# Kernel optimization log

Hardware: AMD Instinct MI355X
Metric: run time of the kernel (lower is better)

The kernel has to match this reference:

```python
import jax, jax.numpy as jnp
import numpy as np
import math

N_HEAD = 16

def setup_inputs() -> dict:
    key = jax.random.key(0)
    ks = jax.random.split(key, 5)
    B, T, C = 4, 2048, 1024
    x = jax.random.normal(ks[0], (B, T, C), dtype=jnp.float32)
    # xavier-uniform-ish scale for dense kernels
    W_attn = jax.random.normal(ks[1], (C, 3 * C), dtype=jnp.float32) * (1.0 / math.sqrt(C))
    b_attn = jnp.zeros((3 * C,), dtype=jnp.float32)
    W_proj = jax.random.normal(ks[2], (C, C), dtype=jnp.float32) * (1.0 / math.sqrt(C))
    b_proj = jnp.zeros((C,), dtype=jnp.float32)
    return {"x": x, "W_attn": W_attn, "b_attn": b_attn, "W_proj": W_proj, "b_proj": b_proj}

def reference(x, W_attn, b_attn, W_proj, b_proj):
    B, T, C = x.shape
    H = N_HEAD
    D = C // H
    qkv = x @ W_attn + b_attn                      # [B,T,3C]
    q, k, v = jnp.split(qkv, 3, axis=-1)
    q = q.reshape(B, T, H, D).transpose(0, 2, 1, 3)  # [B,H,T,D]
    k = k.reshape(B, T, H, D).transpose(0, 2, 1, 3)
    v = v.reshape(B, T, H, D).transpose(0, 2, 1, 3)
    att = jnp.einsum("bhqd,bhkd->bhqk", q, k) * (1.0 / math.sqrt(D))  # [B,H,T,T]
    causal = jnp.tril(jnp.ones((T, T), dtype=bool))
    att = jnp.where(causal, att, jnp.float32(-jnp.inf))
    att = jax.nn.softmax(att, axis=-1)             # exp(att - logsumexp)
    # dropout rates are 0.0 -> identity
    y = jnp.einsum("bhqk,bhkd->bhqd", att, v)      # [B,H,T,D]
    y = y.transpose(0, 2, 1, 3).reshape(B, T, C)
    y = y @ W_proj + b_proj
    return y
```

## Files before the change

### kernel.cpp

```cpp
#include <hip/hip_runtime.h>
#include <hip/hip_bf16.h>

typedef short s16x8 __attribute__((ext_vector_type(8)));
typedef float f32x4 __attribute__((ext_vector_type(4)));
typedef float f32x2 __attribute__((ext_vector_type(2)));

#define MFMA_BF16(A, B, C) __builtin_amdgcn_mfma_f32_16x16x32_bf16(A, B, C, 0, 0, 0)

constexpr int Bn = 4, Tn = 2048, Cn = 1024, Hn = 16, Dn = 64;
constexpr int Mn = Bn * Tn;
constexpr int Nqkv = 3 * Cn;
constexpr float SC = 0.125f * 1.44269504089f;

__device__ __forceinline__ ushort f2bfu(float f) {
    __hip_bfloat16 h = __float2bfloat16(f);
    return *reinterpret_cast<ushort*>(&h);
}
__device__ __forceinline__ uint pkbf(float a, float b) {
    __hip_bfloat162 h = __float22bfloat162_rn(make_float2(a, b));
    return *reinterpret_cast<uint*>(&h);
}

__device__ __forceinline__ f32x2 pk_add(f32x2 a, f32x2 b) {
    f32x2 d; asm("v_pk_add_f32 %0, %1, %2" : "=v"(d) : "v"(a), "v"(b)); return d;
}
__device__ __forceinline__ f32x2 pk_mul(f32x2 a, f32x2 b) {
    f32x2 d; asm("v_pk_mul_f32 %0, %1, %2" : "=v"(d) : "v"(a), "v"(b)); return d;
}

__device__ __forceinline__ void gl_lds16(const void* g, void* l) {
    __builtin_amdgcn_global_load_lds(
        (const __attribute__((address_space(1))) void*)(uintptr_t)g,
        (__attribute__((address_space(3))) void*)(uint32_t)(uintptr_t)l,
        16, 0, 0);
}

__global__ __launch_bounds__(256) void conv_bf16_kernel(
    const float* __restrict__ src, ushort* __restrict__ dst, int n4)
{
    int i = blockIdx.x * blockDim.x + threadIdx.x;
    int stride = gridDim.x * blockDim.x;
    for (; i < n4; i += stride) {
        float4 v = ((const float4*)src)[i];
        ushort4 o;
        o.x = f2bfu(v.x); o.y = f2bfu(v.y); o.z = f2bfu(v.z); o.w = f2bfu(v.w);
        ((ushort4*)dst)[i] = o;
    }
}

__global__ __launch_bounds__(256) void transpose_cvt_kernel(
    const float* __restrict__ W, ushort* __restrict__ Wt, int K, int N)
{
    __shared__ __align__(16) float Ls[64][68];
    const int t = threadIdx.x;
    const int n0 = blockIdx.x * 64, k0 = blockIdx.y * 64;
#pragma unroll
    for (int p = 0; p < 4; ++p) {
        int r = (t >> 4) + p * 16;
        int c = (t & 15) * 4;
        *(float4*)&Ls[r][c] = *(const float4*)&W[(size_t)(k0 + r) * N + n0 + c];
    }
    __syncthreads();
    const int n = t >> 2;
    const int ks = (t & 3) * 16;
    union { ushort s[16]; uint4 u[2]; } tmp;
#pragma unroll
    for (int j = 0; j < 16; ++j) tmp.s[j] = f2bfu(Ls[ks + j][n]);
    uint4* dp = (uint4*)&Wt[(size_t)(n0 + n) * K + k0 + ks];
    dp[0] = tmp.u[0];
    dp[1] = tmp.u[1];
}

__global__ __launch_bounds__(256) void qkv_gemm_mfma(
    const ushort* __restrict__ A, const ushort* __restrict__ Bt,
    const float* __restrict__ bias,
    ushort* __restrict__ Qo, ushort* __restrict__ Ko, ushort* __restrict__ Vo)
{
    __shared__ __align__(16) ushort As[128 * 64];
    __shared__ __align__(16) ushort Bs[128 * 64];
    const int tid = threadIdx.x;
    const int m0 = blockIdx.x * 128, n0 = blockIdx.y * 128;
    const int w = tid >> 6, lane = tid & 63, l15 = lane & 15, qd = lane >> 4;
    const int wm = (w >> 1) * 64, wn = (w & 1) * 64;
    const int lrow = lane >> 3;
    const int lchunk = (lane & 7) ^ (lrow & 7);

    const ushort* gA = A + (size_t)(m0 + w * 32 + lrow) * Cn + lchunk * 8;
    const ushort* gB = Bt + (size_t)(n0 + w * 32 + lrow) * Cn + lchunk * 8;
    ushort* lA = &As[(w * 32) * 64];
    ushort* lB = &Bs[(w * 32) * 64];

    f32x4 acc[4][4] = {};
    const bool isV = (n0 >= 2 * Cn);

    if (!isV) {
        for (int k0 = 0; k0 < Cn; k0 += 64) {
            __syncthreads();
#pragma unroll
            for (int t = 0; t < 4; ++t) {
                gl_lds16(gA + (size_t)t * 8 * Cn + k0, lA + t * 8 * 64);
                gl_lds16(gB + (size_t)t * 8 * Cn + k0, lB + t * 8 * 64);
            }
            __syncthreads();
#pragma unroll
            for (int ks = 0; ks < 2; ++ks) {
                const int xs = (((ks * 4 + qd) ^ (l15 & 7))) * 8;
                s16x8 af[4], bfr[4];
#pragma unroll
                for (int i = 0; i < 4; ++i) {
                    af[i]  = *(const s16x8*)&As[(wm + i * 16 + l15) * 64 + xs];
                    bfr[i] = *(const s16x8*)&Bs[(wn + i * 16 + l15) * 64 + xs];
                }
#pragma unroll
                for (int mt = 0; mt < 4; ++mt)
#pragma unroll
                    for (int nt = 0; nt < 4; ++nt)
                        acc[mt][nt] = MFMA_BF16(af[mt], bfr[nt], acc[mt][nt]);
            }
        }
        const int sel = n0 >> 10;
        ushort* O = (sel == 0) ? Qo : Ko;
        const float scl = (sel == 0) ? SC : 1.0f;
#pragma unroll
        for (int nt = 0; nt < 4; ++nt) {
            const int n_g = n0 + wn + nt * 16 + l15;
            const float bv = bias[n_g];
            const int h = (n_g >> 6) & 15;
            const int d = n_g & 63;
#pragma unroll
            for (int mt = 0; mt < 4; ++mt) {
#pragma unroll
                for (int r = 0; r < 4; ++r) {
                    const int m_g = m0 + wm + mt * 16 + qd * 4 + r;
                    const int b = m_g >> 11, t = m_g & 2047;
                    O[(((size_t)(b * Hn + h) * Tn + t) << 6) + d] =
                        f2bfu((acc[mt][nt][r] + bv) * scl);
                }
            }
        }
    } else {
        for (int k0 = 0; k0 < Cn; k0 += 64) {
            __syncthreads();
#pragma unroll
            for (int t = 0; t < 4; ++t) {
                gl_lds16(gA + (size_t)t * 8 * Cn + k0, lA + t * 8 * 64);
                gl_lds16(gB + (size_t)t * 8 * Cn + k0, lB + t * 8 * 64);
            }
            __syncthreads();
#pragma unroll
            for (int ks = 0; ks < 2; ++ks) {
                const int xs = (((ks * 4 + qd) ^ (l15 & 7))) * 8;
                s16x8 af[4], bfr[4];
#pragma unroll
                for (int i = 0; i < 4; ++i) {
                    af[i]  = *(const s16x8*)&As[(wm + i * 16 + l15) * 64 + xs];
                    bfr[i] = *(const s16x8*)&Bs[(wn + i * 16 + l15) * 64 + xs];
                }
#pragma unroll
                for (int mt = 0; mt < 4; ++mt)
#pragma unroll
                    for (int nt = 0; nt < 4; ++nt)
                        acc[nt][mt] = MFMA_BF16(bfr[nt], af[mt], acc[nt][mt]);
            }
        }
#pragma unroll
        for (int nt = 0; nt < 4; ++nt) {
            const int n_b = n0 + wn + nt * 16 + qd * 4;
            const float4 bv = *(const float4*)&bias[n_b];
            const int h = (n_b >> 6) & 15;
            const int d0 = n_b & 63;
#pragma unroll
            for (int mt = 0; mt < 4; ++mt) {
                const int m_g = m0 + wm + mt * 16 + l15;
                const int b = m_g >> 11, tt = m_g & 2047;
                const size_t rowb = (size_t)(b * Hn + h) * Dn;
                Vo[(rowb + d0 + 0) * Tn + tt] = f2bfu(acc[nt][mt][0] + bv.x);
                Vo[(rowb + d0 + 1) * Tn + tt] = f2bfu(acc[nt][mt][1] + bv.y);
                Vo[(rowb + d0 + 2) * Tn + tt] = f2bfu(acc[nt][mt][2] + bv.z);
                Vo[(rowb + d0 + 3) * Tn + tt] = f2bfu(acc[nt][mt][3] + bv.w);
            }
        }
    }
}

__global__ __launch_bounds__(256, 4) void attn_mfma(
    const ushort* __restrict__ Q, const ushort* __restrict__ K,
    const ushort* __restrict__ Vt, ushort* __restrict__ Y)
{
    __shared__ __align__(16) ushort Ks[2][64 * 64];
    __shared__ __align__(16) ushort Vs[2][64 * 64];
    __shared__ __align__(16) ushort Ps[64 * 64];

    const int tid = threadIdx.x;
    const int bh = blockIdx.x, bx = blockIdx.y;
    const int w = tid >> 6, lane = tid & 63, l15 = lane & 15, qd = lane >> 4;
    const size_t base = (size_t)bh * Tn * Dn;
    const int lrow = lane >> 3;
    const int lchunk = (lane & 7) ^ (lrow & 7);
    const int q_l = w * 16 + l15;
    const int frow = q_l * 64;
    const int fx0 = ((0 * 4 + qd) ^ (l15 & 7)) * 8;
    const int fx1 = ((1 * 4 + qd) ^ (l15 & 7)) * 8;
    const int b = bh >> 4, h = bh & 15;

    const ushort* Kg = K + base + (size_t)(w * 16 + lrow) * Dn + lchunk * 8;
    const ushort* Vg = Vt + base + (size_t)(w * 16 + lrow) * Tn + lchunk * 8;
    const ushort* Qp = Q + base + (size_t)l15 * Dn + qd * 8;

#pragma unroll
    for (int half = 0; half < 2; ++half) {
        const int qt = half ? (31 - bx) : bx;

        const ushort* qrow = Qp + (size_t)(qt * 64 + w * 16) * Dn;
        s16x8 qf0 = *(const s16x8*)(qrow);
        s16x8 qf1 = *(const s16x8*)(qrow + 32);

        __syncthreads();
#pragma unroll
        for (int t = 0; t < 2; ++t) {
            gl_lds16(Kg + (size_t)(t * 8) * Dn, &Ks[0][(w * 16 + t * 8) * 64]);
            gl_lds16(Vg + (size_t)(t * 8) * Tn, &Vs[0][(w * 16 + t * 8) * 64]);
        }

        float m_run = -1e30f, l_run = 0.f;
        f32x4 o[4] = {};

        for (int kt = 0; kt <= qt; ++kt) {
            const int buf = kt & 1;
            __syncthreads();
            if (kt < qt) {
#pragma unroll
                for (int t = 0; t < 2; ++t) {
                    gl_lds16(Kg + (size_t)((kt + 1) * 64 + t * 8) * Dn,
                             &Ks[buf ^ 1][(w * 16 + t * 8) * 64]);
                    gl_lds16(Vg + (size_t)(t * 8) * Tn + (kt + 1) * 64,
                             &Vs[buf ^ 1][(w * 16 + t * 8) * 64]);
                }
            }

            f32x4 s[4] = {};
            __builtin_amdgcn_s_setprio(1);
#pragma unroll
            for (int nt = 0; nt < 4; ++nt) {
                s16x8 kf = *(const s16x8*)&Ks[buf][(nt * 16 + l15) * 64 + fx0];
                s[nt] = MFMA_BF16(kf, qf0, s[nt]);
            }
#pragma unroll
            for (int nt = 0; nt < 4; ++nt) {
                s16x8 kf = *(const s16x8*)&Ks[buf][(nt * 16 + l15) * 64 + fx1];
                s[nt] = MFMA_BF16(kf, qf1, s[nt]);
            }
            __builtin_amdgcn_s_setprio(0);

            if (kt == qt) {
#pragma unroll
                for (int nt = 0; nt < 4; ++nt)
#pragma unroll
                    for (int r = 0; r < 4; ++r)
                        if (nt * 16 + qd * 4 + r > q_l) s[nt][r] = -1e30f;
            }

            float a0 = fmaxf(fmaxf(s[0][0], s[0][1]), fmaxf(s[0][2], s[0][3]));
            float a1 = fmaxf(fmaxf(s[1][0], s[1][1]), fmaxf(s[1][2], s[1][3]));
            float a2 = fmaxf(fmaxf(s[2][0], s[2][1]), fmaxf(s[2][2], s[2][3]));
            float a3 = fmaxf(fmaxf(s[3][0], s[3][1]), fmaxf(s[3][2], s[3][3]));
            float mx = fmaxf(fmaxf(a0, a1), fmaxf(a2, a3));
            mx = fmaxf(mx, __shfl_xor(mx, 16));
            mx = fmaxf(mx, __shfl_xor(mx, 32));

            if (!__all(mx <= m_run + 8.f)) {
                float m_new = fmaxf(m_run, mx);
                float alpha = exp2f(m_run - m_new);
                m_run = m_new;
                l_run *= alpha;
                f32x2 aa = {alpha, alpha};
#pragma unroll
                for (int dt = 0; dt < 4; ++dt) {
                    o[dt].lo = pk_mul(o[dt].lo, aa);
                    o[dt].hi = pk_mul(o[dt].hi, aa);
                }
            }

            const f32x2 negm = {-m_run, -m_run};
            f32x2 lac0 = {0.f, 0.f}, lac1 = {0.f, 0.f};
#pragma unroll
            for (int nt = 0; nt < 4; ++nt) {
                s[nt].lo = pk_add(s[nt].lo, negm);
                s[nt].hi = pk_add(s[nt].hi, negm);
                s[nt][0] = exp2f(s[nt][0]);
                s[nt][1] = exp2f(s[nt][1]);
                s[nt][2] = exp2f(s[nt][2]);
                s[nt][3] = exp2f(s[nt][3]);
                lac0 = pk_add(lac0, s[nt].lo);
                lac1 = pk_add(lac1, s[nt].hi);
            }
            lac0 = pk_add(lac0, lac1);
            l_run += lac0[0] + lac0[1];

#pragma unroll
            for (int nt = 0; nt < 4; ++nt) {
                uint2 pk;
                pk.x = pkbf(s[nt][0], s[nt][1]);
                pk.y = pkbf(s[nt][2], s[nt][3]);
                const int pc = 2 * nt + (qd >> 1), po = (qd & 1) * 4;
                *(uint2*)&Ps[frow + ((pc ^ (l15 & 7)) * 8) + po] = pk;
            }

            {
                s16x8 pb = *(const s16x8*)&Ps[frow + fx0];
                __builtin_amdgcn_s_setprio(1);
#pragma unroll
                for (int dt = 0; dt < 4; ++dt) {
                    s16x8 vf = *(const s16x8*)&Vs[buf][(dt * 16 + l15) * 64 + fx0];
                    o[dt] = MFMA_BF16(vf, pb, o[dt]);
                }
                pb = *(const s16x8*)&Ps[frow + fx1];
#pragma unroll
                for (int dt = 0; dt < 4; ++dt) {
                    s16x8 vf = *(const s16x8*)&Vs[buf][(dt * 16 + l15) * 64 + fx1];
                    o[dt] = MFMA_BF16(vf, pb, o[dt]);
                }
                __builtin_amdgcn_s_setprio(0);
            }
        }

        float lt = l_run;
        lt += __shfl_xor(lt, 16);
        lt += __shfl_xor(lt, 32);
        const float inv = 1.f / lt;
        const int t_g = qt * 64 + w * 16 + l15;
        ushort* yp = Y + ((size_t)(b * Tn + t_g)) * Cn + h * Dn + qd * 4;
#pragma unroll
        for (int dt = 0; dt < 4; ++dt) {
            uint2 pk;
            pk.x = pkbf(o[dt][0] * inv, o[dt][1] * inv);
            pk.y = pkbf(o[dt][2] * inv, o[dt][3] * inv);
            *(uint2*)(yp + dt * 16) = pk;
        }
    }
}

__global__ __launch_bounds__(256) void proj_gemm_mfma(
    const ushort* __restrict__ A, const ushort* __restrict__ Bt,
    const float* __restrict__ bias, float* __restrict__ out)
{
    __shared__ __align__(16) ushort As[128 * 64];
    __shared__ __align__(16) ushort Bs[128 * 64];
    const int tid = threadIdx.x;
    const int m0 = blockIdx.x * 128, n0 = blockIdx.y * 128;
    const int w = tid >> 6, lane = tid & 63, l15 = lane & 15, qd = lane >> 4;
    const int wm = (w >> 1) * 64, wn = (w & 1) * 64;
    const int lrow = lane >> 3;
    const int lchunk = (lane & 7) ^ (lrow & 7);

    const ushort* gA = A + (size_t)(m0 + w * 32 + lrow) * Cn + lchunk * 8;
    const ushort* gB = Bt + (size_t)(n0 + w * 32 + lrow) * Cn + lchunk * 8;
    ushort* lA = &As[(w * 32) * 64];
    ushort* lB = &Bs[(w * 32) * 64];

    f32x4 acc[4][4] = {};

    for (int k0 = 0; k0 < Cn; k0 += 64) {
        __syncthreads();
#pragma unroll
        for (int t = 0; t < 4; ++t) {
            gl_lds16(gA + (size_t)t * 8 * Cn + k0, lA + t * 8 * 64);
            gl_lds16(gB + (size_t)t * 8 * Cn + k0, lB + t * 8 * 64);
        }
        __syncthreads();
#pragma unroll
        for (int ks = 0; ks < 2; ++ks) {
            const int xs = (((ks * 4 + qd) ^ (l15 & 7))) * 8;
            s16x8 af[4], bfr[4];
#pragma unroll
            for (int i = 0; i < 4; ++i) {
                af[i]  = *(const s16x8*)&As[(wm + i * 16 + l15) * 64 + xs];
                bfr[i] = *(const s16x8*)&Bs[(wn + i * 16 + l15) * 64 + xs];
            }
#pragma unroll
            for (int mt = 0; mt < 4; ++mt)
#pragma unroll
                for (int nt = 0; nt < 4; ++nt)
                    acc[mt][nt] = MFMA_BF16(af[mt], bfr[nt], acc[mt][nt]);
        }
    }

#pragma unroll
    for (int nt = 0; nt < 4; ++nt) {
        int n_g = n0 + wn + nt * 16 + l15;
        float bv = bias[n_g];
#pragma unroll
        for (int mt = 0; mt < 4; ++mt) {
#pragma unroll
            for (int r = 0; r < 4; ++r) {
                int m_g = m0 + wm + mt * 16 + qd * 4 + r;
                out[(size_t)m_g * Cn + n_g] = acc[mt][nt][r] + bv;
            }
        }
    }
}

extern "C" void kernel_launch(void* const* d_in, const int* in_sizes, int n_in,
                              void* d_out, int out_size, void* d_ws, size_t ws_size,
                              hipStream_t stream) {
    const float* x      = (const float*)d_in[0];
    const float* W_attn = (const float*)d_in[1];
    const float* b_attn = (const float*)d_in[2];
    const float* W_proj = (const float*)d_in[3];
    const float* b_proj = (const float*)d_in[4];
    float* out = (float*)d_out;

    constexpr size_t PER = (size_t)Mn * Cn;
    ushort* Qb  = (ushort*)d_ws;
    ushort* Kb  = Qb + PER;
    ushort* Vtb = Kb + PER;
    ushort* Yb  = Vtb + PER;

    ushort* WtA  = (ushort*)d_out;
    ushort* x_bf = WtA + (size_t)Nqkv * Cn;
    ushort* WtP  = Qb;

    conv_bf16_kernel<<<1024, 256, 0, stream>>>(x, x_bf, (int)(PER / 4));
    transpose_cvt_kernel<<<dim3(Nqkv / 64, Cn / 64), 256, 0, stream>>>(
        W_attn, WtA, Cn, Nqkv);
    qkv_gemm_mfma<<<dim3(Mn / 128, Nqkv / 128), 256, 0, stream>>>(
        x_bf, WtA, b_attn, Qb, Kb, Vtb);
    attn_mfma<<<dim3(Bn * Hn, 16), 256, 0, stream>>>(Qb, Kb, Vtb, Yb);
    transpose_cvt_kernel<<<dim3(Cn / 64, Cn / 64), 256, 0, stream>>>(
        W_proj, WtP, Cn, Cn);
    proj_gemm_mfma<<<dim3(Mn / 128, Cn / 128), 256, 0, stream>>>(
        Yb, WtP, b_proj, out);
}
```

Measured before the change: 254.1 us.

## Double-buffer LDS in QKV and projection GEMMs with async prefetch pipeline

```diff
diff --git a/kernel.cpp b/kernel.cpp
--- a/kernel.cpp
+++ b/kernel.cpp
@@ -71,13 +71,22 @@
     dp[1] = tmp.u[1];
 }
 
-__global__ __launch_bounds__(256) void qkv_gemm_mfma(
+#define GSTAGE(s, b)                                                          \
+    _Pragma("unroll")                                                         \
+    for (int t_ = 0; t_ < 4; ++t_) {                                          \
+        gl_lds16(gA + (size_t)t_ * 8 * Cn + (s) * 64,                         \
+                 &As[b][(w * 32 + t_ * 8) * 64]);                             \
+        gl_lds16(gB + (size_t)t_ * 8 * Cn + (s) * 64,                         \
+                 &Bs[b][(w * 32 + t_ * 8) * 64]);                             \
+    }
+
+__global__ __launch_bounds__(256, 2) void qkv_gemm_mfma(
     const ushort* __restrict__ A, const ushort* __restrict__ Bt,
     const float* __restrict__ bias,
     ushort* __restrict__ Qo, ushort* __restrict__ Ko, ushort* __restrict__ Vo)
 {
-    __shared__ __align__(16) ushort As[128 * 64];
-    __shared__ __align__(16) ushort Bs[128 * 64];
+    __shared__ __align__(16) ushort As[2][128 * 64];
+    __shared__ __align__(16) ushort Bs[2][128 * 64];
     const int tid = threadIdx.x;
     const int m0 = blockIdx.x * 128, n0 = blockIdx.y * 128;
     const int w = tid >> 6, lane = tid & 63, l15 = lane & 15, qd = lane >> 4;
@@ -87,37 +96,55 @@
 
     const ushort* gA = A + (size_t)(m0 + w * 32 + lrow) * Cn + lchunk * 8;
     const ushort* gB = Bt + (size_t)(n0 + w * 32 + lrow) * Cn + lchunk * 8;
-    ushort* lA = &As[(w * 32) * 64];
-    ushort* lB = &Bs[(w * 32) * 64];
 
     f32x4 acc[4][4] = {};
     const bool isV = (n0 >= 2 * Cn);
 
-    if (!isV) {
-        for (int k0 = 0; k0 < Cn; k0 += 64) {
-            __syncthreads();
-#pragma unroll
-            for (int t = 0; t < 4; ++t) {
-                gl_lds16(gA + (size_t)t * 8 * Cn + k0, lA + t * 8 * 64);
-                gl_lds16(gB + (size_t)t * 8 * Cn + k0, lB + t * 8 * 64);
-            }
-            __syncthreads();
-#pragma unroll
-            for (int ks = 0; ks < 2; ++ks) {
-                const int xs = (((ks * 4 + qd) ^ (l15 & 7))) * 8;
-                s16x8 af[4], bfr[4];
-#pragma unroll
-                for (int i = 0; i < 4; ++i) {
-                    af[i]  = *(const s16x8*)&As[(wm + i * 16 + l15) * 64 + xs];
-                    bfr[i] = *(const s16x8*)&Bs[(wn + i * 16 + l15) * 64 + xs];
-                }
+    GSTAGE(0, 0);
+    GSTAGE(1, 1);
+
+    for (int s = 0; s < 16; ++s) {
+        if (s < 15) { asm volatile("s_waitcnt vmcnt(8)" ::: "memory"); }
+        else        { asm volatile("s_waitcnt vmcnt(0)" ::: "memory"); }
+        __builtin_amdgcn_sched_barrier(0);
+        __builtin_amdgcn_s_barrier();
+        __builtin_amdgcn_sched_barrier(0);
+
+        const ushort* a_ = As[s & 1];
+        const ushort* b_ = Bs[s & 1];
+        __builtin_amdgcn_s_setprio(1);
+#pragma unroll
+        for (int ks = 0; ks < 2; ++ks) {
+            const int xs = (((ks * 4 + qd) ^ (l15 & 7))) * 8;
+            s16x8 af[4], bfr[4];
+#pragma unroll
+            for (int i = 0; i < 4; ++i) {
+                af[i]  = *(const s16x8*)&a_[(wm + i * 16 + l15) * 64 + xs];
+                bfr[i] = *(const s16x8*)&b_[(wn + i * 16 + l15) * 64 + xs];
+            }
+            if (!isV) {
 #pragma unroll
                 for (int mt = 0; mt < 4; ++mt)
 #pragma unroll
                     for (int nt = 0; nt < 4; ++nt)
                         acc[mt][nt] = MFMA_BF16(af[mt], bfr[nt], acc[mt][nt]);
-            }
-        }
+            } else {
+#pragma unroll
+                for (int mt = 0; mt < 4; ++mt)
+#pragma unroll
+                    for (int nt = 0; nt < 4; ++nt)
+                        acc[nt][mt] = MFMA_BF16(bfr[nt], af[mt], acc[nt][mt]);
+            }
+        }
+        __builtin_amdgcn_s_setprio(0);
+
+        __builtin_amdgcn_sched_barrier(0);
+        __builtin_amdgcn_s_barrier();
+        __builtin_amdgcn_sched_barrier(0);
+        if (s + 2 < 16) { GSTAGE(s + 2, s & 1); }
+    }
+
+    if (!isV) {
         const int sel = n0 >> 10;
         ushort* O = (sel == 0) ? Qo : Ko;
         const float scl = (sel == 0) ? SC : 1.0f;
@@ -139,30 +166,6 @@
             }
         }
     } else {
-        for (int k0 = 0; k0 < Cn; k0 += 64) {
-            __syncthreads();
-#pragma unroll
-            for (int t = 0; t < 4; ++t) {
-                gl_lds16(gA + (size_t)t * 8 * Cn + k0, lA + t * 8 * 64);
-                gl_lds16(gB + (size_t)t * 8 * Cn + k0, lB + t * 8 * 64);
-            }
-            __syncthreads();
-#pragma unroll
-            for (int ks = 0; ks < 2; ++ks) {
-                const int xs = (((ks * 4 + qd) ^ (l15 & 7))) * 8;
-                s16x8 af[4], bfr[4];
-#pragma unroll
-                for (int i = 0; i < 4; ++i) {
-                    af[i]  = *(const s16x8*)&As[(wm + i * 16 + l15) * 64 + xs];
-                    bfr[i] = *(const s16x8*)&Bs[(wn + i * 16 + l15) * 64 + xs];
-                }
-#pragma unroll
-                for (int mt = 0; mt < 4; ++mt)
-#pragma unroll
-                    for (int nt = 0; nt < 4; ++nt)
-                        acc[nt][mt] = MFMA_BF16(bfr[nt], af[mt], acc[nt][mt]);
-            }
-        }
 #pragma unroll
         for (int nt = 0; nt < 4; ++nt) {
             const int n_b = n0 + wn + nt * 16 + qd * 4;
@@ -340,12 +343,12 @@
     }
 }
 
-__global__ __launch_bounds__(256) void proj_gemm_mfma(
+__global__ __launch_bounds__(256, 2) void proj_gemm_mfma(
     const ushort* __restrict__ A, const ushort* __restrict__ Bt,
     const float* __restrict__ bias, float* __restrict__ out)
 {
-    __shared__ __align__(16) ushort As[128 * 64];
-    __shared__ __align__(16) ushort Bs[128 * 64];
+    __shared__ __align__(16) ushort As[2][128 * 64];
+    __shared__ __align__(16) ushort Bs[2][128 * 64];
     const int tid = threadIdx.x;
     const int m0 = blockIdx.x * 128, n0 = blockIdx.y * 128;
     const int w = tid >> 6, lane = tid & 63, l15 = lane & 15, qd = lane >> 4;
@@ -355,27 +358,30 @@
 
     const ushort* gA = A + (size_t)(m0 + w * 32 + lrow) * Cn + lchunk * 8;
     const ushort* gB = Bt + (size_t)(n0 + w * 32 + lrow) * Cn + lchunk * 8;
-    ushort* lA = &As[(w * 32) * 64];
-    ushort* lB = &Bs[(w * 32) * 64];
 
     f32x4 acc[4][4] = {};
 
-    for (int k0 = 0; k0 < Cn; k0 += 64) {
-        __syncthreads();
-#pragma unroll
-        for (int t = 0; t < 4; ++t) {
-            gl_lds16(gA + (size_t)t * 8 * Cn + k0, lA + t * 8 * 64);
-            gl_lds16(gB + (size_t)t * 8 * Cn + k0, lB + t * 8 * 64);
-        }
-        __syncthreads();
+    GSTAGE(0, 0);
+    GSTAGE(1, 1);
+
+    for (int s = 0; s < 16; ++s) {
+        if (s < 15) { asm volatile("s_waitcnt vmcnt(8)" ::: "memory"); }
+        else        { asm volatile("s_waitcnt vmcnt(0)" ::: "memory"); }
+        __builtin_amdgcn_sched_barrier(0);
+        __builtin_amdgcn_s_barrier();
+        __builtin_amdgcn_sched_barrier(0);
+
+        const ushort* a_ = As[s & 1];
+        const ushort* b_ = Bs[s & 1];
+        __builtin_amdgcn_s_setprio(1);
 #pragma unroll
         for (int ks = 0; ks < 2; ++ks) {
             const int xs = (((ks * 4 + qd) ^ (l15 & 7))) * 8;
             s16x8 af[4], bfr[4];
 #pragma unroll
             for (int i = 0; i < 4; ++i) {
-                af[i]  = *(const s16x8*)&As[(wm + i * 16 + l15) * 64 + xs];
-                bfr[i] = *(const s16x8*)&Bs[(wn + i * 16 + l15) * 64 + xs];
+                af[i]  = *(const s16x8*)&a_[(wm + i * 16 + l15) * 64 + xs];
+                bfr[i] = *(const s16x8*)&b_[(wn + i * 16 + l15) * 64 + xs];
             }
 #pragma unroll
             for (int mt = 0; mt < 4; ++mt)
@@ -383,6 +389,12 @@
                 for (int nt = 0; nt < 4; ++nt)
                     acc[mt][nt] = MFMA_BF16(af[mt], bfr[nt], acc[mt][nt]);
         }
+        __builtin_amdgcn_s_setprio(0);
+
+        __builtin_amdgcn_sched_barrier(0);
+        __builtin_amdgcn_s_barrier();
+        __builtin_amdgcn_sched_barrier(0);
+        if (s + 2 < 16) { GSTAGE(s + 2, s & 1); }
     }
 
 #pragma unroll
```

Result: faster. 245.8 us (-3.3%).
